# Optimization experiments

Measured on AMD Instinct MI355X. Metric: run time of the kernel, lower is better.

Reference implementation:

```python
import jax, jax.numpy as jnp
import numpy as np

N = 100000
E = 3200000
IN_C = 512
HID = 64
LOC = 64
GLOB = 64
OUT_C = 40
K = 10
ALPHA = 0.1


def setup_inputs() -> dict:
    key = jax.random.key(0)
    ks = jax.random.split(key, 10)
    batch_x = jax.random.normal(ks[0], (N, IN_C), dtype=jnp.float32)
    edge_index = jax.random.randint(ks[1], (2, E), 0, N, dtype=jnp.int32)
    glob_emb = jax.random.normal(ks[2], (N, GLOB), dtype=jnp.float32)
    # Linear params (Glorot-ish scale)
    W1 = jax.random.normal(ks[3], (IN_C, HID), dtype=jnp.float32) / np.sqrt(IN_C)
    b1 = jnp.zeros((HID,), dtype=jnp.float32)
    W2 = jax.random.normal(ks[4], (HID, LOC), dtype=jnp.float32) / np.sqrt(HID)
    b2 = jnp.zeros((LOC,), dtype=jnp.float32)
    # GPR-GNN PPR init coefficients: temp[k] = alpha*(1-alpha)^k, temp[K] = (1-alpha)^K
    temp_np = ALPHA * (1.0 - ALPHA) ** np.arange(K + 1)
    temp_np[-1] = (1.0 - ALPHA) ** K
    temp = jnp.asarray(temp_np, dtype=jnp.float32)
    Wl = jax.random.normal(ks[5], (LOC + GLOB, OUT_C), dtype=jnp.float32) / np.sqrt(LOC + GLOB)
    bl = jnp.zeros((OUT_C,), dtype=jnp.float32)
    return {"batch_x": batch_x, "edge_index": edge_index, "glob_emb": glob_emb,
            "W1": W1, "b1": b1, "W2": W2, "b2": b2, "temp": temp, "Wl": Wl, "bl": bl}


def _gcn_norm(edge_index, num_nodes):
    # add self loops (weight 1), symmetric normalization like PyG gcn_norm
    loops = jnp.arange(num_nodes, dtype=edge_index.dtype)
    row = jnp.concatenate([edge_index[0], loops])  # sources
    col = jnp.concatenate([edge_index[1], loops])  # targets
    w = jnp.ones(row.shape[0], dtype=jnp.float32)
    deg = jax.ops.segment_sum(w, col, num_segments=num_nodes)
    dinv = jnp.where(deg > 0, jax.lax.rsqrt(jnp.maximum(deg, 1.0)), 0.0)
    norm = dinv[row] * dinv[col]
    return row, col, norm


def reference(batch_x, edge_index, glob_emb, W1, b1, W2, b2, temp, Wl, bl):
    # eval mode: all dropouts are identity
    x = jax.nn.relu(batch_x @ W1 + b1)
    x = x @ W2 + b2  # [N, LOC]
    n = x.shape[0]
    row, col, norm = _gcn_norm(edge_index, n)
    hidden = x * temp[0]
    for k in range(K):
        # message: norm * x[src]; aggregate: scatter-add at target
        x = jax.ops.segment_sum(norm[:, None] * x[row], col, num_segments=n)
        hidden = hidden + temp[k + 1] * x
    emb = jnp.concatenate([hidden, glob_emb], axis=1)  # [N, LOC+GLOB]
    return emb @ Wl + bl
```

## Files before the change

kernel.cpp:

```cpp
#include <hip/hip_runtime.h>


typedef _Float16 half8 __attribute__((ext_vector_type(8)));


__global__ __launch_bounds__(256) void count_kernel(const int* __restrict__ edge,
                                                    int* __restrict__ counts, int E) {
  int e = blockIdx.x * 256 + threadIdx.x;
  if (e < E) atomicAdd(&counts[edge[E + e]], 1);
}

__global__ __launch_bounds__(256) void scanA_kernel(const int* __restrict__ counts,
                                                    int* __restrict__ incl,
                                                    int* __restrict__ partials, int Nn) {
  __shared__ int sbuf[256];
  int t = threadIdx.x;
  int base = blockIdx.x * 1024 + t * 4;
  int a0 = (base + 0 < Nn) ? counts[base + 0] : 0;
  int a1 = (base + 1 < Nn) ? counts[base + 1] : 0;
  int a2 = (base + 2 < Nn) ? counts[base + 2] : 0;
  int a3 = (base + 3 < Nn) ? counts[base + 3] : 0;
  int tot = a0 + a1 + a2 + a3;
  sbuf[t] = tot;
  __syncthreads();
  for (int off = 1; off < 256; off <<= 1) {
    int v = (t >= off) ? sbuf[t - off] : 0;
    __syncthreads();
    sbuf[t] += v;
    __syncthreads();
  }
  int excl = sbuf[t] - tot;
  if (base + 0 < Nn) incl[base + 0] = excl + a0;
  if (base + 1 < Nn) incl[base + 1] = excl + a0 + a1;
  if (base + 2 < Nn) incl[base + 2] = excl + a0 + a1 + a2;
  if (base + 3 < Nn) incl[base + 3] = excl + tot;
  if (t == 255) partials[blockIdx.x] = sbuf[255];
}

__global__ void scanB_kernel(const int* __restrict__ partials,
                             int* __restrict__ chunkoff, int B) {
  __shared__ int sbuf[256];
  int t = threadIdx.x;
  int v = (t < B) ? partials[t] : 0;
  sbuf[t] = v;
  __syncthreads();
  for (int off = 1; off < 256; off <<= 1) {
    int u = (t >= off) ? sbuf[t - off] : 0;
    __syncthreads();
    sbuf[t] += u;
    __syncthreads();
  }
  chunkoff[t] = sbuf[t] - v;
}

__global__ __launch_bounds__(256) void finalize_scan_kernel(const int* __restrict__ incl,
                                                            const int* __restrict__ chunkoff,
                                                            int* __restrict__ rowptr, int Nn) {
  int i = blockIdx.x * 256 + threadIdx.x;
  if (i < Nn) rowptr[i + 1] = incl[i] + chunkoff[i >> 10];
  if (i == 0) rowptr[0] = 0;
}

__global__ __launch_bounds__(256) void dinv_kernel(const int* __restrict__ counts,
                                                   float* __restrict__ dinv, int Nn) {
  int i = blockIdx.x * 256 + threadIdx.x;
  if (i < Nn) dinv[i] = rsqrtf((float)(counts[i] + 1));
}

__global__ __launch_bounds__(256) void fill_kernel(const int* __restrict__ edge,
                                                   const int* __restrict__ rowptr,
                                                   int* __restrict__ cursor,
                                                   int* __restrict__ srcoff, int E) {
  int e = blockIdx.x * 256 + threadIdx.x;
  if (e < E) {
    int r = edge[e];
    int c = edge[E + e];
    int p = rowptr[c] + atomicAdd(&cursor[c], 1);
    srcoff[p] = r * 128;
  }
}


__global__ __launch_bounds__(256) void mlp1_kernel(const float* __restrict__ X,
                                                   const float* __restrict__ W1,
                                                   const float* __restrict__ b1,
                                                   float* __restrict__ H, int Nn) {
  __shared__ float sXT[64][68];
  __shared__ float sW[64][68];
  int t = threadIdx.x;
  int m0 = blockIdx.x * 64;
  int tx = t & 15, ty = t >> 4;
  float acc[4][4];
#pragma unroll
  for (int i = 0; i < 4; ++i)
#pragma unroll
    for (int j = 0; j < 4; ++j) acc[i][j] = 0.f;

  for (int k0 = 0; k0 < 512; k0 += 64) {
#pragma unroll
    for (int i = 0; i < 4; ++i) {
      int lin = t + i * 256;
      int m = lin >> 4;
      int kq = lin & 15;
      int gr = m0 + m;
      float4 v = make_float4(0.f, 0.f, 0.f, 0.f);
      if (gr < Nn) v = *(const float4*)&X[(size_t)gr * 512 + k0 + kq * 4];
      sXT[kq * 4 + 0][m] = v.x;
      sXT[kq * 4 + 1][m] = v.y;
      sXT[kq * 4 + 2][m] = v.z;
      sXT[kq * 4 + 3][m] = v.w;
    }
#pragma unroll
    for (int i = 0; i < 4; ++i) {
      int lin = t + i * 256;
      int k = lin >> 4;
      int nq = lin & 15;
      float4 v = *(const float4*)&W1[(size_t)(k0 + k) * 64 + nq * 4];
      *(float4*)&sW[k][nq * 4] = v;
    }
    __syncthreads();
#pragma unroll 8
    for (int kk = 0; kk < 64; ++kk) {
      float4 a = *(const float4*)&sXT[kk][ty * 4];
      float4 b = *(const float4*)&sW[kk][tx * 4];
      float av[4] = {a.x, a.y, a.z, a.w};
      float bv[4] = {b.x, b.y, b.z, b.w};
#pragma unroll
      for (int i = 0; i < 4; ++i)
#pragma unroll
        for (int j = 0; j < 4; ++j) acc[i][j] += av[i] * bv[j];
    }
    __syncthreads();
  }
  float4 bb = *(const float4*)&b1[tx * 4];
  float bvv[4] = {bb.x, bb.y, bb.z, bb.w};
#pragma unroll
  for (int i = 0; i < 4; ++i) {
    int r = m0 + ty * 4 + i;
    if (r < Nn) {
      float4 o;
      o.x = fmaxf(acc[i][0] + bvv[0], 0.f);
      o.y = fmaxf(acc[i][1] + bvv[1], 0.f);
      o.z = fmaxf(acc[i][2] + bvv[2], 0.f);
      o.w = fmaxf(acc[i][3] + bvv[3], 0.f);
      *(float4*)&H[(size_t)r * 64 + tx * 4] = o;
    }
  }
}


__global__ void computeM_kernel(const float* __restrict__ W2, const float* __restrict__ Wl,
                                const float* __restrict__ b2, float* __restrict__ Mm,
                                float* __restrict__ cv) {
  int t = threadIdx.x;
  for (int idx = t; idx < 2560; idx += 256) {
    int k = idx / 40, o = idx - k * 40;
    float s = 0.f;
    for (int j = 0; j < 64; ++j) s += W2[k * 64 + j] * Wl[j * 40 + o];
    Mm[idx] = s;
  }
  if (t < 40) {
    float s = 0.f;
    for (int j = 0; j < 64; ++j) s += b2[j] * Wl[j * 40 + t];
    cv[t] = s;
  }
}

__global__ void zeropad_kernel(char* __restrict__ yA, char* __restrict__ yB, int Nn) {
  int t = threadIdx.x;
  ((_Float16*)(yA + (size_t)Nn * 128))[t] = (_Float16)0.f;
  ((_Float16*)(yB + (size_t)Nn * 128))[t] = (_Float16)0.f;
}


__global__ __launch_bounds__(256) void z0_kernel(const float* __restrict__ H,
                                                 const float* __restrict__ Mm,
                                                 const float* __restrict__ cv,
                                                 const float* __restrict__ dinv,
                                                 const float* __restrict__ temp,
                                                 char* __restrict__ y0,
                                                 float* __restrict__ hid, int Nn) {
  __shared__ float sM[2624];
  __shared__ float sc[40];
  int t = threadIdx.x;
  for (int i = t; i < 2560; i += 256) sM[i] = Mm[i];
  for (int i = 2560 + t; i < 2624; i += 256) sM[i] = 0.f;
  if (t < 40) sc[t] = cv[t];
  __syncthreads();
  int wid = t >> 6, lane = t & 63;
  int node = blockIdx.x * 4 + wid;
  if (node < Nn) {
    float h = H[(size_t)node * 64 + lane];
    float acc = (lane < 40) ? sc[lane] : 0.f;
#pragma unroll 8
    for (int k = 0; k < 64; ++k) acc += __shfl(h, k) * sM[k * 40 + lane];
    if (lane < 40) {
      float di = dinv[node];
      float y = di * acc;
      ((_Float16*)(y0 + (size_t)node * 128))[lane] = (_Float16)y;
      hid[(size_t)node * 40 + lane] = temp[0] * y;
    }
  }
}


__global__ __launch_bounds__(256) void prop_kernel(const char* __restrict__ yin,
                                                   char* __restrict__ yout,
                                                   float* __restrict__ hid,
                                                   const int* __restrict__ srcoff,
                                                   const int* __restrict__ rowptr,
                                                   const float* __restrict__ dinv,
                                                   const float* __restrict__ temp,
                                                   int kidx, int Nn) {
  __shared__ float red[4][60][8];
  int t = threadIdx.x, wid = t >> 6, lane = t & 63;
  int node = blockIdx.x * 4 + wid;
  int sub = lane / 5;
  int cl = lane - sub * 5;
  const int zoff = Nn * 128;
  float a0 = 0.f, a1 = 0.f, a2 = 0.f, a3 = 0.f, a4 = 0.f, a5 = 0.f, a6 = 0.f, a7 = 0.f;
  if (node < Nn) {
    int start = rowptr[node], end = rowptr[node + 1];
    int claneoff = cl << 4;
    for (int b0 = start; b0 < end; b0 += 60) {
      int j = b0 + lane;
      int moff = (lane < 60 && j < end) ? srcoff[j] : zoff;
#pragma unroll
      for (int tt = 0; tt < 5; ++tt) {
        int off = __shfl(moff, tt * 12 + sub);
        half8 v = *(const half8*)(yin + off + claneoff);
        a0 += (float)v[0]; a1 += (float)v[1]; a2 += (float)v[2]; a3 += (float)v[3];
        a4 += (float)v[4]; a5 += (float)v[5]; a6 += (float)v[6]; a7 += (float)v[7];
      }
    }
  }
  if (lane < 60) {
    red[wid][lane][0] = a0; red[wid][lane][1] = a1;
    red[wid][lane][2] = a2; red[wid][lane][3] = a3;
    red[wid][lane][4] = a4; red[wid][lane][5] = a5;
    red[wid][lane][6] = a6; red[wid][lane][7] = a7;
  }
  __syncthreads();
  if (node < Nn && lane < 5) {
    float s[8];
#pragma unroll
    for (int i = 0; i < 8; ++i) s[i] = 0.f;
#pragma unroll
    for (int g = 0; g < 12; ++g)
#pragma unroll
      for (int i = 0; i < 8; ++i) s[i] += red[wid][g * 5 + lane][i];
    float di = dinv[node];
    float m = di * di;
    half8 self = *(const half8*)(yin + (size_t)node * 128 + (lane << 4));
    float yn[8];
    half8 outv;
#pragma unroll
    for (int i = 0; i < 8; ++i) {
      yn[i] = m * (s[i] + (float)self[i]);
      outv[i] = (_Float16)yn[i];
    }
    *(half8*)(yout + (size_t)node * 128 + (lane << 4)) = outv;
    float tk = temp[kidx];
    float* hp = &hid[(size_t)node * 40 + lane * 8];
    float4 h0 = *(float4*)hp;
    float4 h1 = *(float4*)(hp + 4);
    h0.x += tk * yn[0]; h0.y += tk * yn[1]; h0.z += tk * yn[2]; h0.w += tk * yn[3];
    h1.x += tk * yn[4]; h1.y += tk * yn[5]; h1.z += tk * yn[6]; h1.w += tk * yn[7];
    *(float4*)hp = h0;
    *(float4*)(hp + 4) = h1;
  }
}


__global__ __launch_bounds__(256) void final_kernel(const float* __restrict__ glob,
                                                    const float* __restrict__ Wl,
                                                    const float* __restrict__ bl,
                                                    const float* __restrict__ hid,
                                                    const int* __restrict__ counts,
                                                    const float* __restrict__ dinv,
                                                    float* __restrict__ out, int Nn) {
  __shared__ float sW[2624];
  __shared__ float sb[40];
  int t = threadIdx.x;
  for (int i = t; i < 2560; i += 256) sW[i] = Wl[2560 + i];
  for (int i = 2560 + t; i < 2624; i += 256) sW[i] = 0.f;
  if (t < 40) sb[t] = bl[t];
  __syncthreads();
  int wid = t >> 6, lane = t & 63;
  int node = blockIdx.x * 4 + wid;
  if (node < Nn) {
    float g = glob[(size_t)node * 64 + lane];
    float acc = (lane < 40) ? sb[lane] : 0.f;
#pragma unroll 8
    for (int k = 0; k < 64; ++k) acc += __shfl(g, k) * sW[k * 40 + lane];
    if (lane < 40) {
      float sc = (float)(counts[node] + 1) * dinv[node];
      out[(size_t)node * 40 + lane] = sc * hid[(size_t)node * 40 + lane] + acc;
    }
  }
}


extern "C" void kernel_launch(void* const* d_in, const int* in_sizes, int n_in,
                              void* d_out, int out_size, void* d_ws, size_t ws_size,
                              hipStream_t stream) {
  const float* X    = (const float*)d_in[0];
  const int*   edge = (const int*)d_in[1];
  const float* glob = (const float*)d_in[2];
  const float* W1   = (const float*)d_in[3];
  const float* b1   = (const float*)d_in[4];
  const float* W2   = (const float*)d_in[5];
  const float* b2   = (const float*)d_in[6];
  const float* temp = (const float*)d_in[7];
  const float* Wl   = (const float*)d_in[8];
  const float* bl   = (const float*)d_in[9];
  float* out = (float*)d_out;

  int Nn = in_sizes[0] / 512;
  int E  = in_sizes[1] / 2;
  int Kk = in_sizes[7] - 1;

  char* p = (char*)d_ws;
  auto alloc = [&](size_t bytes) {
    char* r = p;
    p += (bytes + 255) & ~(size_t)255;
    return r;
  };
  int*   counts   = (int*)alloc((size_t)Nn * 4);
  int*   rowptr   = (int*)alloc((size_t)(Nn + 1) * 4);
  int*   incl     = (int*)alloc((size_t)Nn * 4);
  int*   partials = (int*)alloc(256 * 4);
  int*   chunkoff = (int*)alloc(256 * 4);
  int*   cursor   = (int*)alloc((size_t)Nn * 4);
  float* dinv     = (float*)alloc((size_t)Nn * 4);
  int*   srcoff   = (int*)alloc((size_t)E * 4);
  float* Hbuf     = (float*)alloc((size_t)Nn * 64 * 4);
  float* Mm       = (float*)alloc(2560 * 4);
  float* cv       = (float*)alloc(64 * 4);
  char*  yA       = (char*)alloc((size_t)(Nn + 1) * 128);
  char*  yB       = (char*)alloc((size_t)(Nn + 1) * 128);
  float* hid      = (float*)alloc((size_t)Nn * 40 * 4);

  hipMemsetAsync(counts, 0, (size_t)Nn * 4, stream);
  hipMemsetAsync(cursor, 0, (size_t)Nn * 4, stream);

  count_kernel<<<(E + 255) / 256, 256, 0, stream>>>(edge, counts, E);
  int B = (Nn + 1023) / 1024;
  scanA_kernel<<<B, 256, 0, stream>>>(counts, incl, partials, Nn);
  scanB_kernel<<<1, 256, 0, stream>>>(partials, chunkoff, B);
  finalize_scan_kernel<<<(Nn + 255) / 256, 256, 0, stream>>>(incl, chunkoff, rowptr, Nn);
  dinv_kernel<<<(Nn + 255) / 256, 256, 0, stream>>>(counts, dinv, Nn);
  fill_kernel<<<(E + 255) / 256, 256, 0, stream>>>(edge, rowptr, cursor, srcoff, E);

  mlp1_kernel<<<(Nn + 63) / 64, 256, 0, stream>>>(X, W1, b1, Hbuf, Nn);
  computeM_kernel<<<1, 256, 0, stream>>>(W2, Wl, b2, Mm, cv);
  zeropad_kernel<<<1, 64, 0, stream>>>(yA, yB, Nn);

  int nodeBlocks = (Nn + 3) / 4;
  z0_kernel<<<nodeBlocks, 256, 0, stream>>>(Hbuf, Mm, cv, dinv, temp, yA, hid, Nn);

  char* yin = yA;
  char* yout = yB;
  for (int k = 1; k <= Kk; ++k) {
    prop_kernel<<<nodeBlocks, 256, 0, stream>>>(yin, yout, hid, srcoff, rowptr, dinv,
                                                temp, k, Nn);
    char* tmpp = yin; yin = yout; yout = tmpp;
  }

  final_kernel<<<nodeBlocks, 256, 0, stream>>>(glob, Wl, bl, hid, counts, dinv, out, Nn);
}
```

Before: 1.409 ms.

## Bucket edges by destination range before CSR fill to localize atomics and scatters

Adds a bucketing pass that groups packed (dst,src) edge pairs into 49 destination-range buckets of 2048 nodes, using shared-memory counters and one global atomic per bucket per block. The fill step then walks each bucket in chunks, so cursor atomics and srcoff writes touch a narrow, cache-resident region instead of random spots across the whole array. Block indices are interleaved so that concurrent blocks work on different buckets. The cost is an extra read and write of the whole edge list as 8-byte pairs, plus a fixed per-bucket capacity that could overflow with skewed degree distributions.

```diff
diff --git a/kernel.cpp b/kernel.cpp
--- a/kernel.cpp
+++ b/kernel.cpp
@@ -8,6 +8,65 @@
                                                     int* __restrict__ counts, int E) {
   int e = blockIdx.x * 256 + threadIdx.x;
   if (e < E) atomicAdd(&counts[edge[E + e]], 1);
+}
+
+__global__ __launch_bounds__(256) void bucketA_kernel(const int* __restrict__ edge,
+                                                      unsigned long long* __restrict__ barr,
+                                                      int* __restrict__ bcnt,
+                                                      int E, int cap) {
+  __shared__ int lcnt[64];
+  __shared__ int lbase[64];
+  int t = threadIdx.x;
+  if (t < 64) lcnt[t] = 0;
+  __syncthreads();
+  int e0 = blockIdx.x * 2048 + t;
+  int rk[8];
+  int bk[8];
+  unsigned long long pk[8];
+#pragma unroll
+  for (int i = 0; i < 8; ++i) {
+    int e = e0 + i * 256;
+    int s = 0, c = 0;
+    if (e < E) { s = edge[e]; c = edge[E + e]; }
+    int b = c >> 11;
+    bk[i] = b;
+    pk[i] = ((unsigned long long)(unsigned)c << 32) | (unsigned)s;
+    if (e < E) rk[i] = atomicAdd(&lcnt[b], 1);
+    else rk[i] = -1;
+  }
+  __syncthreads();
+  if (t < 64 && lcnt[t] > 0) lbase[t] = atomicAdd(&bcnt[t], lcnt[t]);
+  __syncthreads();
+#pragma unroll
+  for (int i = 0; i < 8; ++i)
+    if (rk[i] >= 0)
+      barr[(size_t)bk[i] * cap + lbase[bk[i]] + rk[i]] = pk[i];
+}
+
+__global__ __launch_bounds__(256) void fillB_kernel(const unsigned long long* __restrict__ barr,
+                                                    const int* __restrict__ bcnt,
+                                                    const int* __restrict__ rowptr,
+                                                    int* __restrict__ cursor,
+                                                    int* __restrict__ srcoff,
+                                                    int cap, int nb, int nbx, int cpb) {
+  int i = blockIdx.x;
+  int x = i & 7;
+  int j = i >> 3;
+  int bslot = j % nbx;
+  int chunk = j / nbx;
+  int b = x + 8 * bslot;
+  if (b >= nb) return;
+  int cnt = bcnt[b];
+  int lo = (int)((long long)cnt * chunk / cpb);
+  int hi = (int)((long long)cnt * (chunk + 1) / cpb);
+  const unsigned long long* ep = barr + (size_t)b * cap;
+  for (int e = lo + threadIdx.x; e < hi; e += 256) {
+    unsigned long long pk = ep[e];
+    int s = (int)(unsigned)pk;
+    int c = (int)(pk >> 32);
+    int p = rowptr[c] + atomicAdd(&cursor[c], 1);
+    srcoff[p] = s * 128;
+  }
 }
 
 __global__ __launch_bounds__(256) void scanA_kernel(const int* __restrict__ counts,
@@ -65,19 +124,6 @@
                                                    float* __restrict__ dinv, int Nn) {
   int i = blockIdx.x * 256 + threadIdx.x;
   if (i < Nn) dinv[i] = rsqrtf((float)(counts[i] + 1));
-}
-
-__global__ __launch_bounds__(256) void fill_kernel(const int* __restrict__ edge,
-                                                   const int* __restrict__ rowptr,
-                                                   int* __restrict__ cursor,
-                                                   int* __restrict__ srcoff, int E) {
-  int e = blockIdx.x * 256 + threadIdx.x;
-  if (e < E) {
-    int r = edge[e];
-    int c = edge[E + e];
-    int p = rowptr[c] + atomicAdd(&cursor[c], 1);
-    srcoff[p] = r * 128;
-  }
 }
 
 
@@ -341,16 +387,26 @@
   char*  yB       = (char*)alloc((size_t)(Nn + 1) * 128);
   float* hid      = (float*)alloc((size_t)Nn * 40 * 4);
 
+  int nb  = (Nn + 2047) >> 11;
+  int nbx = (nb + 7) / 8;
+  int cap = E / nb + E / (nb * 8) + 1024;
+  unsigned long long* barr = (unsigned long long*)alloc((size_t)nb * cap * 8);
+  int* bcnt = (int*)alloc(64 * 4);
+
   hipMemsetAsync(counts, 0, (size_t)Nn * 4, stream);
   hipMemsetAsync(cursor, 0, (size_t)Nn * 4, stream);
+  hipMemsetAsync(bcnt, 0, 64 * 4, stream);
 
   count_kernel<<<(E + 255) / 256, 256, 0, stream>>>(edge, counts, E);
+  bucketA_kernel<<<(E + 2047) / 2048, 256, 0, stream>>>(edge, barr, bcnt, E, cap);
   int B = (Nn + 1023) / 1024;
   scanA_kernel<<<B, 256, 0, stream>>>(counts, incl, partials, Nn);
   scanB_kernel<<<1, 256, 0, stream>>>(partials, chunkoff, B);
   finalize_scan_kernel<<<(Nn + 255) / 256, 256, 0, stream>>>(incl, chunkoff, rowptr, Nn);
   dinv_kernel<<<(Nn + 255) / 256, 256, 0, stream>>>(counts, dinv, Nn);
-  fill_kernel<<<(E + 255) / 256, 256, 0, stream>>>(edge, rowptr, cursor, srcoff, E);
+  int cpb = 32;
+  fillB_kernel<<<8 * nbx * cpb, 256, 0, stream>>>(barr, bcnt, rowptr, cursor, srcoff,
+                                                  cap, nb, nbx, cpb);
 
   mlp1_kernel<<<(Nn + 63) / 64, 256, 0, stream>>>(X, W1, b1, Hbuf, Nn);
   computeM_kernel<<<1, 256, 0, stream>>>(W2, Wl, b2, Mm, cv);
```

Result: no change. 1.415 ms (+0.5%).
